# Optimization experiments

Measured on AMD Instinct MI355X. Metric: run time of the kernel, lower is better.

Reference implementation:

```python
import jax, jax.numpy as jnp
import numpy as np
import math

B, S, D, L, FF = 16, 2048, 512, 4, 2048
VOCAB, ATTR_VOCAB, MAXPOS = 33, 608, 2048
EPS = 1e-5


def layernorm(x, w, b):
    mu = jnp.mean(x, axis=-1, keepdims=True)
    var = jnp.mean(jnp.square(x - mu), axis=-1, keepdims=True)
    return (x - mu) * jax.lax.rsqrt(var + EPS) * w + b


def setup_inputs() -> dict:
    key = jax.random.key(0)
    ks = jax.random.split(key, 16)
    std = 0.02
    return {
        "input_ids": jax.random.randint(ks[0], (B, S), 0, VOCAB),
        "combined_indices": jax.random.randint(ks[1], (B,), 0, ATTR_VOCAB),
        "attention_mask": jnp.ones((B, S), dtype=jnp.float32),
        "tok_emb": jax.random.normal(ks[2], (VOCAB, D), jnp.float32) * std,
        "pos_emb": jax.random.normal(ks[3], (MAXPOS, D), jnp.float32) * std,
        "attr_emb": jax.random.normal(ks[4], (ATTR_VOCAB, D), jnp.float32) * std,
        "ln_w": jnp.ones((L, D), jnp.float32),
        "ln_b": jnp.zeros((L, D), jnp.float32),
        "w1": jax.random.normal(ks[5], (L, D, FF), jnp.float32) * std,
        "b1": jnp.zeros((L, FF), jnp.float32),
        "w2": jax.random.normal(ks[6], (L, FF, D), jnp.float32) * std,
        "b2": jnp.zeros((L, D), jnp.float32),
        "out_w": jax.random.normal(ks[7], (D, VOCAB), jnp.float32) * std,
        "out_b": jnp.zeros((VOCAB,), jnp.float32),
    }


def reference(input_ids, combined_indices, attention_mask, tok_emb, pos_emb,
              attr_emb, ln_w, ln_b, w1, b1, w2, b2, out_w, out_b):
    scale = 1.0 / math.sqrt(D)
    # embeddings: token + position + per-example attribute (broadcast over seq)
    x = tok_emb[input_ids] + pos_emb[jnp.arange(S)][None, :, :] \
        + attr_emb[combined_indices][:, None, :]
    mask_add = (1.0 - attention_mask)[:, None, :] * -1e9  # [B,1,S]
    for l in range(L):
        h = layernorm(x, ln_w[l], ln_b[l])                 # shared LN params used twice
        scores = jnp.einsum('bsd,btd->bst', h, h) * scale + mask_add
        probs = jax.nn.softmax(scores, axis=-1)            # dropout=0 (eval)
        attn = jnp.einsum('bst,btd->bsd', probs, h) + x    # residual
        n2 = layernorm(attn, ln_w[l], ln_b[l])
        ff = jax.nn.gelu(n2 @ w1[l] + b1[l], approximate=False) @ w2[l] + b2[l]
        x = ff + attn
    return x @ out_w + out_b
```

## Files before the change

### kernel.cpp

```cpp
#include <hip/hip_runtime.h>
#include <hip/hip_bf16.h>
#include <cmath>

#define B_ 16
#define S_ 2048
#define D_ 512
#define L_ 4
#define FF_ 2048
#define V_ 33

typedef unsigned short u16;
typedef __attribute__((ext_vector_type(8))) short bf16x8;
typedef __attribute__((ext_vector_type(4))) float f32x4;

__device__ __forceinline__ u16 f2bf(float f) {
    unsigned x = __float_as_uint(f);
    unsigned r = (x + 0x7fffu + ((x >> 16) & 1u)) >> 16;
    return (u16)r;
}
__device__ __forceinline__ float bf2f(u16 u) { return __uint_as_float(((unsigned)u) << 16); }

__device__ __forceinline__ float wave_sum(float v) {
#pragma unroll
    for (int o = 32; o; o >>= 1) v += __shfl_xor(v, o);
    return v;
}

__device__ __forceinline__ void gload16(const u16* g, u16* l) {
    __builtin_amdgcn_global_load_lds((const __attribute__((address_space(1))) void*)g,
                                     (__attribute__((address_space(3))) void*)l, 16, 0, 0);
}

__device__ __forceinline__ uint4 pack8(const u16* ov) {
    uint4 p;
    p.x = (unsigned)ov[0] | ((unsigned)ov[1] << 16);
    p.y = (unsigned)ov[2] | ((unsigned)ov[3] << 16);
    p.z = (unsigned)ov[4] | ((unsigned)ov[5] << 16);
    p.w = (unsigned)ov[6] | ((unsigned)ov[7] << 16);
    return p;
}

__global__ __launch_bounds__(256) void embed_kernel(
    const int* __restrict__ ids, const int* __restrict__ attr,
    const float* __restrict__ tok, const float* __restrict__ pos,
    const float* __restrict__ attre, u16* __restrict__ x)
{
    int idx = blockIdx.x * 256 + threadIdx.x;
    const int total = B_ * S_ * (D_ / 8);
    if (idx >= total) return;
    int d8 = idx & (D_ / 8 - 1);
    int bs = idx >> 6;
    int s  = bs & (S_ - 1);
    int b  = bs >> 11;
    int id = ids[bs];
    int a  = attr[b];
    const float4* t4 = (const float4*)(tok   + (size_t)id * D_) + d8 * 2;
    const float4* p4 = (const float4*)(pos   + (size_t)s  * D_) + d8 * 2;
    const float4* a4 = (const float4*)(attre + (size_t)a  * D_) + d8 * 2;
    u16 ov[8];
#pragma unroll
    for (int h = 0; h < 2; h++) {
        float4 t = t4[h], p = p4[h], at = a4[h];
        ov[h * 4 + 0] = f2bf(t.x + p.x + at.x);
        ov[h * 4 + 1] = f2bf(t.y + p.y + at.y);
        ov[h * 4 + 2] = f2bf(t.z + p.z + at.z);
        ov[h * 4 + 3] = f2bf(t.w + p.w + at.w);
    }
    *(uint4*)(x + (size_t)idx * 8) = pack8(ov);
}

__global__ __launch_bounds__(256) void ln_kernel(
    const u16* __restrict__ in, u16* __restrict__ out,
    const float* __restrict__ w, const float* __restrict__ b, int rows)
{
    int gw = (int)((blockIdx.x * 256 + threadIdx.x) >> 6);
    int lane = threadIdx.x & 63;
    if (gw >= rows) return;
    uint4 pk = *(const uint4*)(in + (size_t)gw * D_ + lane * 8);
    float xv[8];
    xv[0] = bf2f((u16)(pk.x & 0xffff)); xv[1] = bf2f((u16)(pk.x >> 16));
    xv[2] = bf2f((u16)(pk.y & 0xffff)); xv[3] = bf2f((u16)(pk.y >> 16));
    xv[4] = bf2f((u16)(pk.z & 0xffff)); xv[5] = bf2f((u16)(pk.z >> 16));
    xv[6] = bf2f((u16)(pk.w & 0xffff)); xv[7] = bf2f((u16)(pk.w >> 16));
    float s = 0.f;
#pragma unroll
    for (int k = 0; k < 8; k++) s += xv[k];
    s = wave_sum(s);
    float mu = s * (1.f / D_);
    float q = 0.f;
#pragma unroll
    for (int k = 0; k < 8; k++) { float d = xv[k] - mu; q += d * d; }
    q = wave_sum(q);
    float rs = rsqrtf(q * (1.f / D_) + 1e-5f);
    const float4* w4 = (const float4*)w;
    const float4* b4 = (const float4*)b;
    float4 w0 = w4[lane * 2], w1v = w4[lane * 2 + 1];
    float4 b0 = b4[lane * 2], b1v = b4[lane * 2 + 1];
    float wv[8] = {w0.x, w0.y, w0.z, w0.w, w1v.x, w1v.y, w1v.z, w1v.w};
    float bv[8] = {b0.x, b0.y, b0.z, b0.w, b1v.x, b1v.y, b1v.z, b1v.w};
    u16 ov[8];
#pragma unroll
    for (int k = 0; k < 8; k++) ov[k] = f2bf((xv[k] - mu) * rs * wv[k] + bv[k]);
    *(uint4*)(out + (size_t)gw * D_ + lane * 8) = pack8(ov);
}

#define LTS 66
__global__ __launch_bounds__(1024) void lnT_kernel(
    const u16* __restrict__ in, u16* __restrict__ h, u16* __restrict__ hT,
    const float* __restrict__ w, const float* __restrict__ b)
{
    __shared__ u16 tile[512 * LTS];
    const int tid = threadIdx.x, lane = tid & 63, wv = tid >> 6;
    const int rb = blockIdx.x;
    const int z  = rb >> 5;
    const int s0 = (rb & 31) * 64;

    float wv8[8], bv8[8];
#pragma unroll
    for (int k = 0; k < 8; k++) {
        wv8[k] = w[k * 64 + lane];
        bv8[k] = b[k * 64 + lane];
    }

#pragma unroll
    for (int i = 0; i < 4; i++) {
        const int rl = wv * 4 + i;
        const size_t grow = (size_t)rb * 64 + rl;
        const u16* xr = in + grow * D_;
        float xv[8];
#pragma unroll
        for (int k = 0; k < 8; k++) xv[k] = bf2f(xr[k * 64 + lane]);
        float s = 0.f;
#pragma unroll
        for (int k = 0; k < 8; k++) s += xv[k];
        s = wave_sum(s);
        float mu = s * (1.f / D_);
        float q = 0.f;
#pragma unroll
        for (int k = 0; k < 8; k++) { float d = xv[k] - mu; q += d * d; }
        q = wave_sum(q);
        float rs = rsqrtf(q * (1.f / D_) + 1e-5f);
        u16* hr = h + grow * D_;
#pragma unroll
        for (int k = 0; k < 8; k++) {
            u16 v = f2bf((xv[k] - mu) * rs * wv8[k] + bv8[k]);
            hr[k * 64 + lane] = v;
            tile[(k * 64 + lane) * LTS + rl] = v;
        }
    }
    __syncthreads();
    u16* hb = hT + (size_t)z * S_ * D_;
#pragma unroll
    for (int it = 0; it < 4; it++) {
        int idx = it * 1024 + tid;
        int d = idx >> 3, sg = (idx & 7) << 3;
        u16 v[8];
#pragma unroll
        for (int i = 0; i < 8; i++) v[i] = tile[d * LTS + sg + i];
        *(uint4*)(hb + (size_t)d * S_ + s0 + sg) = pack8(v);
    }
}

__device__ __forceinline__ void ld2(const float* p, int idx, u16& a, u16& b) {
    float2 v = ((const float2*)p)[idx];
    a = f2bf(v.x); b = f2bf(v.y);
}

__global__ void transpose64(const float* __restrict__ in, u16* __restrict__ out,
                            int R, int C, size_t sIn, size_t sOut)
{
    __shared__ u16 tile[64][66];
    const float* ip = in + (size_t)blockIdx.z * sIn;
    u16* op = out + (size_t)blockIdx.z * sOut;
    const int tx = threadIdx.x, ty = threadIdx.y;
#pragma unroll
    for (int i = 0; i < 8; i++) {
        int r = blockIdx.y * 64 + ty + i * 8;
        u16 a, b;
        ld2(ip + (size_t)r * C, blockIdx.x * 32 + tx, a, b);
        tile[tx * 2 + 0][ty + i * 8] = a;
        tile[tx * 2 + 1][ty + i * 8] = b;
    }
    __syncthreads();
#pragma unroll
    for (int i = 0; i < 8; i++) {
        int ocl = ty + i * 8;
        int oc  = blockIdx.x * 64 + ocl;
        unsigned w = (unsigned)tile[ocl][tx * 2] | ((unsigned)tile[ocl][tx * 2 + 1] << 16);
        ((unsigned*)(op + (size_t)oc * R + blockIdx.y * 64))[tx] = w;
    }
}

enum { E_PV = 1, E_GELU = 2, E_FF2 = 3 };

template <int EPI>
__global__ __launch_bounds__(256) void gemm_nt(
    const u16* __restrict__ A, size_t sAz, int lda,
    const u16* __restrict__ B, size_t sBz, int ldb,
    u16* Cb, size_t sCz, int ldc,
    int K,
    const u16* resid, size_t sRz,
    const float* __restrict__ bias,
    const float* __restrict__ aux, int b0)
{
    __shared__ __align__(16) u16 ldsA[128 * 64];
    __shared__ __align__(16) u16 ldsB[128 * 64];
    __shared__ float l2[EPI == E_PV ? 128 : 1][2];

    const int gx = gridDim.x, gy = gridDim.y;
    const int nwg = gx * gy * gridDim.z;
    int lid = blockIdx.x + gx * (blockIdx.y + gy * blockIdx.z);
    {
        const int q = nwg >> 3, r = nwg & 7;
        const int xcd = lid & 7, idx = lid >> 3;
        lid = (xcd < r ? xcd * (q + 1) : r * (q + 1) + (xcd - r) * q) + idx;
    }
    const int bx = lid % gx;
    const int t2 = lid / gx;
    const int by = t2 % gy;
    const int z  = t2 / gy;

    A += (size_t)z * sAz;
    B += (size_t)z * sBz;
    const size_t coff = (size_t)z * sCz;
    const int brow = by * 128, bcol = bx * 128;
    const int tid = threadIdx.x, lane = tid & 63, wid = tid >> 6;
    const int wr = wid >> 1, wc = wid & 1;

    if constexpr (EPI == E_PV) {
        const int nrows = b0;
        const int base = z * S_ + brow;
        const int r = tid >> 1, ih = (tid & 1) << 4;
        float s = 0.f;
#pragma unroll
        for (int i = 0; i < 16; i++)
            s += aux[(size_t)(ih + i) * nrows + base + r];
        l2[r][tid & 1] = s;
    }

    f32x4 acc[4][4];
#pragma unroll
    for (int m = 0; m < 4; m++)
#pragma unroll
        for (int n = 0; n < 4; n++) acc[m][n] = 0.0f;

    const int lg   = lane >> 3;
    const int srow = wid * 8 + lg;
    const int skk  = ((lane & 7) ^ lg) << 3;
    const int l15 = lane & 15, l7 = lane & 7, kh = lane >> 4;

    for (int k0 = 0; k0 < K; k0 += 64) {
        __syncthreads();
#pragma unroll
        for (int r = 0; r < 4; r++) {
            const u16* ga = A + (size_t)(brow + r * 32 + srow) * lda + (k0 + skk);
            const u16* gb = B + (size_t)(bcol + r * 32 + srow) * ldb + (k0 + skk);
            gload16(ga, &ldsA[r * 2048 + wid * 512]);
            gload16(gb, &ldsB[r * 2048 + wid * 512]);
        }
        __syncthreads();
#pragma unroll
        for (int kk = 0; kk < 64; kk += 32) {
            const int kc = (kk >> 3) + kh;
            const int kswz = ((kc ^ l7) << 3);
            bf16x8 af[4], bfv[4];
#pragma unroll
            for (int m = 0; m < 4; m++)
                af[m] = *(const bf16x8*)&ldsA[(wr * 64 + m * 16 + l15) * 64 + kswz];
#pragma unroll
            for (int n = 0; n < 4; n++)
                bfv[n] = *(const bf16x8*)&ldsB[(wc * 64 + n * 16 + l15) * 64 + kswz];
#pragma unroll
            for (int m = 0; m < 4; m++)
#pragma unroll
                for (int n = 0; n < 4; n++)
                    acc[m][n] = __builtin_amdgcn_mfma_f32_16x16x32_bf16(af[m], bfv[n], acc[m][n], 0, 0, 0);
        }
    }

#pragma unroll
    for (int m = 0; m < 4; m++)
#pragma unroll
        for (int n = 0; n < 4; n++) {
            int rowb = brow + wr * 64 + m * 16 + ((lane >> 4) << 2);
            int col  = bcol + wc * 64 + n * 16 + l15;
#pragma unroll
            for (int j = 0; j < 4; j++) {
                int row = rowb + j;
                float v = acc[m][n][j];
                size_t off = coff + (size_t)row * ldc + col;
                if constexpr (EPI == E_PV) {
                    int rl = row - brow;
                    float lv = l2[rl][0] + l2[rl][1];
                    Cb[off] = f2bf(v / lv +
                                   bf2f(resid[(size_t)z * sRz + (size_t)row * ldc + col]));
                } else if constexpr (EPI == E_GELU) {
                    float t = v + bias[col];
                    Cb[off] = f2bf(0.5f * t * (1.f + erff(t * 0.70710678118f)));
                } else {
                    Cb[off] = f2bf(v + bias[col] +
                                   bf2f(resid[(size_t)row * ldc + col]));
                }
            }
        }
}

__global__ __launch_bounds__(256) void gemm_sc(
    const u16* __restrict__ h, u16* __restrict__ P,
    const float* __restrict__ mask, int b0, float scale,
    float* __restrict__ psum, int nbatch)
{
    __shared__ __align__(16) u16 ldsbuf[2][128 * 64];
    u16* ldsA = ldsbuf[0];
    u16* ldsB = ldsbuf[1];
    u16* mt   = &ldsbuf[0][0];

    const int nwg = 136 * nbatch;
    int lid = blockIdx.x + 136 * blockIdx.z;
    {
        const int q = nwg >> 3, r = nwg & 7;
        const int xcd = lid & 7, idx = lid >> 3;
        lid = (xcd < r ? xcd * (q + 1) : r * (q + 1) + (xcd - r) * q) + idx;
    }
    int t = lid % 136;
    const int z = lid / 136;
    int by = 0;
#pragma unroll 1
    while (t >= 16 - by) { t -= 16 - by; by++; }
    const int bx = by + t;

    const u16* A = h + (size_t)z * S_ * D_;
    const size_t coff = (size_t)z * S_ * S_;
    const int brow = by * 128, bcol = bx * 128;
    const int tid = threadIdx.x, lane = tid & 63, wid = tid >> 6;
    const int wr = wid >> 1, wc = wid & 1;

    f32x4 acc[4][4];
#pragma unroll
    for (int m = 0; m < 4; m++)
#pragma unroll
        for (int n = 0; n < 4; n++) acc[m][n] = 0.0f;

    const int lg   = lane >> 3;
    const int srow = wid * 8 + lg;
    const int skk  = ((lane & 7) ^ lg) << 3;
    const int l15 = lane & 15, l7 = lane & 7, kh = lane >> 4;

    for (int k0 = 0; k0 < D_; k0 += 64) {
        __syncthreads();
#pragma unroll
        for (int r = 0; r < 4; r++) {
            const u16* ga = A + (size_t)(brow + r * 32 + srow) * D_ + (k0 + skk);
            const u16* gb = A + (size_t)(bcol + r * 32 + srow) * D_ + (k0 + skk);
            gload16(ga, &ldsA[r * 2048 + wid * 512]);
            gload16(gb, &ldsB[r * 2048 + wid * 512]);
        }
        __syncthreads();
#pragma unroll
        for (int kk = 0; kk < 64; kk += 32) {
            const int kc = (kk >> 3) + kh;
            const int kswz = ((kc ^ l7) << 3);
            bf16x8 af[4], bfv[4];
#pragma unroll
            for (int m = 0; m < 4; m++)
                af[m] = *(const bf16x8*)&ldsA[(wr * 64 + m * 16 + l15) * 64 + kswz];
#pragma unroll
            for (int n = 0; n < 4; n++)
                bfv[n] = *(const bf16x8*)&ldsB[(wc * 64 + n * 16 + l15) * 64 + kswz];
#pragma unroll
            for (int m = 0; m < 4; m++)
#pragma unroll
                for (int n = 0; n < 4; n++)
                    acc[m][n] = __builtin_amdgcn_mfma_f32_16x16x32_bf16(af[m], bfv[n], acc[m][n], 0, 0, 0);
        }
    }

    const float* mrow = mask + (size_t)(b0 + z) * S_;
    const int nrows = nbatch * S_;

    float rsum[4][4];
#pragma unroll
    for (int m = 0; m < 4; m++)
#pragma unroll
        for (int j = 0; j < 4; j++) rsum[m][j] = 0.f;

#pragma unroll
    for (int m = 0; m < 4; m++)
#pragma unroll
        for (int n = 0; n < 4; n++) {
            int rowb = brow + wr * 64 + m * 16 + (kh << 2);
            int col  = bcol + wc * 64 + n * 16 + l15;
            float madd_c = (1.f - mrow[col]) * -1e9f;
#pragma unroll
            for (int j = 0; j < 4; j++) {
                int row = rowb + j;
                float ev = __expf(acc[m][n][j] * scale + madd_c);
                P[coff + (size_t)row * S_ + col] = f2bf(ev);
                rsum[m][j] += ev;
            }
        }
#pragma unroll
    for (int m = 0; m < 4; m++) {
        int rowl = brow + wr * 64 + m * 16 + (kh << 2);
#pragma unroll
        for (int j = 0; j < 4; j++) {
            float s = rsum[m][j];
            s += __shfl_xor(s, 1);
            s += __shfl_xor(s, 2);
            s += __shfl_xor(s, 4);
            s += __shfl_xor(s, 8);
            if (l15 == 0)
                psum[(size_t)(bx * 2 + wc) * nrows + (size_t)z * S_ + rowl + j] = s;
        }
    }

    if (bx != by) {
#pragma unroll 1
        for (int rnd = 0; rnd < 2; rnd++) {
            __syncthreads();
            if (wc == rnd) {
#pragma unroll
                for (int n = 0; n < 4; n++) {
                    float csum = 0.f;
                    const int mrow_l = n * 16 + l15;
#pragma unroll
                    for (int m = 0; m < 4; m++) {
                        const int lr = wr * 64 + m * 16 + (kh << 2);
                        u16 e2[4];
#pragma unroll
                        for (int j = 0; j < 4; j++) {
                            float madd_r = (1.f - mrow[brow + lr + j]) * -1e9f;
                            float em = __expf(acc[m][n][j] * scale + madd_r);
                            csum += em;
                            e2[j] = f2bf(em);
                        }
                        unsigned* m32 = (unsigned*)&mt[mrow_l * 136 + lr];
                        m32[0] = (unsigned)e2[0] | ((unsigned)e2[1] << 16);
                        m32[1] = (unsigned)e2[2] | ((unsigned)e2[3] << 16);
                    }
                    csum += __shfl_xor(csum, 16);
                    csum += __shfl_xor(csum, 32);
                    if (lane < 16)
                        psum[(size_t)(by * 2 + wr) * nrows + (size_t)z * S_ +
                             bcol + rnd * 64 + n * 16 + lane] = csum;
                }
            }
            __syncthreads();
#pragma unroll 1
            for (int i = tid; i < 64 * 16; i += 256) {
                int rr = i >> 4, c16 = (i & 15) << 3;
                u16 v[8];
#pragma unroll
                for (int q = 0; q < 8; q++) v[q] = mt[rr * 136 + c16 + q];
                *(uint4*)(P + coff + (size_t)(bcol + rnd * 64 + rr) * S_ + brow + c16) = pack8(v);
            }
        }
    }
}

__global__ __launch_bounds__(256) void wtb_kernel(
    const float* __restrict__ W, u16* __restrict__ WTb)
{
    int i = blockIdx.x * 256 + threadIdx.x;
    if (i >= 64 * 512) return;
    int n = i >> 9, k = i & 511;
    WTb[i] = f2bf(n < V_ ? W[k * V_ + n] : 0.f);
}

__global__ __launch_bounds__(256) void outproj_mfma(
    const u16* __restrict__ x, const u16* __restrict__ WTb,
    const float* __restrict__ bias, float* __restrict__ out)
{
    __shared__ __align__(16) u16 ldsA[128 * 64];
    __shared__ __align__(16) u16 ldsB[64 * 64];
    __shared__ float obuf[128][34];
    const int brow = blockIdx.x * 128;
    const int tid = threadIdx.x, lane = tid & 63, wid = tid >> 6;
    const int wr = wid >> 1, wc = wid & 1;
    const int l15 = lane & 15, l7 = lane & 7, kh = lane >> 4;
    const int lg = lane >> 3, srow = wid * 8 + lg;
    const int skk = ((lane & 7) ^ lg) << 3;

    f32x4 acc[4][2];
#pragma unroll
    for (int m = 0; m < 4; m++)
#pragma unroll
        for (int n = 0; n < 2; n++) acc[m][n] = 0.0f;

    for (int k0 = 0; k0 < 512; k0 += 64) {
        __syncthreads();
#pragma unroll
        for (int r = 0; r < 2; r++)
            gload16(WTb + (size_t)(r * 32 + srow) * 512 + (k0 + skk),
                    &ldsB[r * 2048 + wid * 512]);
#pragma unroll
        for (int r = 0; r < 4; r++)
            gload16(x + (size_t)(brow + r * 32 + srow) * 512 + (k0 + skk),
                    &ldsA[r * 2048 + wid * 512]);
        __syncthreads();
#pragma unroll
        for (int kk = 0; kk < 64; kk += 32) {
            const int kc = (kk >> 3) + kh;
            const int kswz = ((kc ^ l7) << 3);
            bf16x8 af[4], bfv[2];
#pragma unroll
            for (int m = 0; m < 4; m++)
                af[m] = *(const bf16x8*)&ldsA[(wr * 64 + m * 16 + l15) * 64 + kswz];
#pragma unroll
            for (int n = 0; n < 2; n++)
                bfv[n] = *(const bf16x8*)&ldsB[(wc * 32 + n * 16 + l15) * 64 + kswz];
#pragma unroll
            for (int m = 0; m < 4; m++)
#pragma unroll
                for (int n = 0; n < 2; n++)
                    acc[m][n] = __builtin_amdgcn_mfma_f32_16x16x32_bf16(af[m], bfv[n], acc[m][n], 0, 0, 0);
        }
    }

#pragma unroll
    for (int m = 0; m < 4; m++)
#pragma unroll
        for (int n = 0; n < 2; n++) {
            int rowl = wr * 64 + m * 16 + ((lane >> 4) << 2);
            int col  = wc * 32 + n * 16 + l15;
            if (col < V_) {
#pragma unroll
                for (int j = 0; j < 4; j++)
                    obuf[rowl + j][col] = acc[m][n][j] + bias[col];
            }
        }
    __syncthreads();
    float* ob = out + (size_t)brow * V_;
#pragma unroll 1
    for (int i = tid; i < 128 * V_; i += 256)
        ob[i] = obuf[i / V_][i % V_];
}

extern "C" void kernel_launch(void* const* d_in, const int* in_sizes, int n_in,
                              void* d_out, int out_size, void* d_ws, size_t ws_size,
                              hipStream_t stream)
{
    const int*   input_ids = (const int*)d_in[0];
    const int*   comb      = (const int*)d_in[1];
    const float* amask     = (const float*)d_in[2];
    const float* tok       = (const float*)d_in[3];
    const float* pos       = (const float*)d_in[4];
    const float* attre     = (const float*)d_in[5];
    const float* ln_w      = (const float*)d_in[6];
    const float* ln_b      = (const float*)d_in[7];
    const float* w1        = (const float*)d_in[8];
    const float* b1        = (const float*)d_in[9];
    const float* w2        = (const float*)d_in[10];
    const float* b2        = (const float*)d_in[11];
    const float* out_w     = (const float*)d_in[12];
    const float* out_b     = (const float*)d_in[13];
    float* out = (float*)d_out;
    (void)in_sizes; (void)n_in; (void)out_size;

    int NB_A, RC;
    if      (ws_size >= 300000000ULL) { NB_A = 16; RC = 32768; }
    else if (ws_size >= 180000000ULL) { NB_A = 8;  RC = 16384; }
    else if (ws_size >= 120000000ULL) { NB_A = 4;  RC = 8192;  }
    else                              { NB_A = 2;  RC = 4096;  }
    const int HR = NB_A * S_;

    unsigned char* ws = (unsigned char*)d_ws;
    size_t off = 0;
    auto carve = [&](size_t bytes) {
        void* p = ws + off;
        off += (bytes + 255) & ~(size_t)255;
        return p;
    };
    u16* x      = (u16*)carve((size_t)B_ * S_ * D_ * 2);
    u16* w1t    = (u16*)carve((size_t)L_ * D_ * FF_ * 2);
    u16* w2t    = (u16*)carve((size_t)L_ * D_ * FF_ * 2);
    u16* h      = (u16*)carve((size_t)HR * D_ * 2);
    u16* hT     = (u16*)carve((size_t)NB_A * S_ * D_ * 2);
    float* psum = (float*)carve((size_t)NB_A * S_ * 32 * 4);
    u16* WTb    = (u16*)carve((size_t)64 * 512 * 2);
    size_t scP_bytes  = (size_t)NB_A * S_ * S_ * 2;
    size_t tbuf_bytes = (size_t)RC * FF_ * 2;
    void* un = carve(scP_bytes > tbuf_bytes ? scP_bytes : tbuf_bytes);
    u16* scP  = (u16*)un;
    u16* tbuf = (u16*)un;

    const float scl = 1.0f / sqrtf((float)D_);
    const int nG = B_ / NB_A;
    const int nC = (B_ * S_) / RC;

    embed_kernel<<<(B_ * S_ * (D_ / 8)) / 256, 256, 0, stream>>>(input_ids, comb, tok, pos, attre, x);
    transpose64<<<dim3(FF_ / 64, D_ / 64, L_), dim3(32, 8), 0, stream>>>(
        w1, w1t, D_, FF_, (size_t)D_ * FF_, (size_t)FF_ * D_);
    transpose64<<<dim3(D_ / 64, FF_ / 64, L_), dim3(32, 8), 0, stream>>>(
        w2, w2t, FF_, D_, (size_t)FF_ * D_, (size_t)D_ * FF_);
    wtb_kernel<<<128, 256, 0, stream>>>(out_w, WTb);

    for (int l = 0; l < L_; l++) {
        const float* lw = ln_w + l * D_;
        const float* lb = ln_b + l * D_;

        for (int g = 0; g < nG; g++) {
            u16* xg = x + (size_t)g * NB_A * S_ * D_;
            lnT_kernel<<<(NB_A * S_) / 64, 1024, 0, stream>>>(xg, h, hT, lw, lb);
            gemm_sc<<<dim3(136, 1, NB_A), 256, 0, stream>>>(
                h, scP, amask, g * NB_A, scl, psum, NB_A);
            gemm_nt<E_PV><<<dim3(D_ / 128, S_ / 128, NB_A), 256, 0, stream>>>(
                scP, (size_t)S_ * S_, S_,
                hT, (size_t)S_ * D_, S_,
                xg, (size_t)S_ * D_, D_,
                S_, xg, (size_t)S_ * D_, nullptr, psum, NB_A * S_);
        }

        for (int c = 0; c < nC; c++) {
            size_t roff = (size_t)c * RC;
            ln_kernel<<<RC / 4, 256, 0, stream>>>(x + roff * D_, h, lw, lb, RC);
            gemm_nt<E_GELU><<<dim3(FF_ / 128, RC / 128, 1), 256, 0, stream>>>(
                h, 0, D_,
                w1t + (size_t)l * FF_ * D_, 0, D_,
                tbuf, 0, FF_,
                D_, nullptr, 0, b1 + l * FF_, nullptr, 0);
            gemm_nt<E_FF2><<<dim3(D_ / 128, RC / 128, 1), 256, 0, stream>>>(
                tbuf, 0, FF_,
                w2t + (size_t)l * D_ * FF_, 0, FF_,
                x + roff * D_, 0, D_,
                FF_, x + roff * D_, 0, b2 + l * D_, nullptr, 0);
        }
    }

    outproj_mfma<<<(B_ * S_) / 128, 256, 0, stream>>>(x, WTb, out_b, out);
}
```

Before: 1.905 ms.

## Fuse second LayerNorm into FF1 GEMM prologue

Drops the standalone LayerNorm kernel before the first feed-forward GEMM and builds a dedicated FF1 GEMM that computes per-row mean and variance itself. It then normalizes the A tile on the fly while staging it into LDS. This removes one kernel launch and the write and re-read of the normalized activation buffer. In exchange, every column block recomputes row statistics and the normalization (16x redundant across FF/128 blocks). The A tile is now loaded synchronously through registers rather than with async global-to-LDS loads, and variance uses the one-pass E[x²]-mu² form, which is less accurate.

```diff
diff --git a/kernel.cpp b/kernel.cpp
--- a/kernel.cpp
+++ b/kernel.cpp
@@ -38,6 +38,12 @@
     p.z = (unsigned)ov[4] | ((unsigned)ov[5] << 16);
     p.w = (unsigned)ov[6] | ((unsigned)ov[7] << 16);
     return p;
+}
+__device__ __forceinline__ void unpack8(uint4 p, float* v) {
+    v[0] = bf2f((u16)(p.x & 0xffff)); v[1] = bf2f((u16)(p.x >> 16));
+    v[2] = bf2f((u16)(p.y & 0xffff)); v[3] = bf2f((u16)(p.y >> 16));
+    v[4] = bf2f((u16)(p.z & 0xffff)); v[5] = bf2f((u16)(p.z >> 16));
+    v[6] = bf2f((u16)(p.w & 0xffff)); v[7] = bf2f((u16)(p.w >> 16));
 }
 
 __global__ __launch_bounds__(256) void embed_kernel(
@@ -69,41 +75,6 @@
     *(uint4*)(x + (size_t)idx * 8) = pack8(ov);
 }
 
-__global__ __launch_bounds__(256) void ln_kernel(
-    const u16* __restrict__ in, u16* __restrict__ out,
-    const float* __restrict__ w, const float* __restrict__ b, int rows)
-{
-    int gw = (int)((blockIdx.x * 256 + threadIdx.x) >> 6);
-    int lane = threadIdx.x & 63;
-    if (gw >= rows) return;
-    uint4 pk = *(const uint4*)(in + (size_t)gw * D_ + lane * 8);
-    float xv[8];
-    xv[0] = bf2f((u16)(pk.x & 0xffff)); xv[1] = bf2f((u16)(pk.x >> 16));
-    xv[2] = bf2f((u16)(pk.y & 0xffff)); xv[3] = bf2f((u16)(pk.y >> 16));
-    xv[4] = bf2f((u16)(pk.z & 0xffff)); xv[5] = bf2f((u16)(pk.z >> 16));
-    xv[6] = bf2f((u16)(pk.w & 0xffff)); xv[7] = bf2f((u16)(pk.w >> 16));
-    float s = 0.f;
-#pragma unroll
-    for (int k = 0; k < 8; k++) s += xv[k];
-    s = wave_sum(s);
-    float mu = s * (1.f / D_);
-    float q = 0.f;
-#pragma unroll
-    for (int k = 0; k < 8; k++) { float d = xv[k] - mu; q += d * d; }
-    q = wave_sum(q);
-    float rs = rsqrtf(q * (1.f / D_) + 1e-5f);
-    const float4* w4 = (const float4*)w;
-    const float4* b4 = (const float4*)b;
-    float4 w0 = w4[lane * 2], w1v = w4[lane * 2 + 1];
-    float4 b0 = b4[lane * 2], b1v = b4[lane * 2 + 1];
-    float wv[8] = {w0.x, w0.y, w0.z, w0.w, w1v.x, w1v.y, w1v.z, w1v.w};
-    float bv[8] = {b0.x, b0.y, b0.z, b0.w, b1v.x, b1v.y, b1v.z, b1v.w};
-    u16 ov[8];
-#pragma unroll
-    for (int k = 0; k < 8; k++) ov[k] = f2bf((xv[k] - mu) * rs * wv[k] + bv[k]);
-    *(uint4*)(out + (size_t)gw * D_ + lane * 8) = pack8(ov);
-}
-
 #define LTS 66
 __global__ __launch_bounds__(1024) void lnT_kernel(
     const u16* __restrict__ in, u16* __restrict__ h, u16* __restrict__ hT,
@@ -191,7 +162,7 @@
     }
 }
 
-enum { E_PV = 1, E_GELU = 2, E_FF2 = 3 };
+enum { E_PV = 1, E_FF2 = 3 };
 
 template <int EPI>
 __global__ __launch_bounds__(256) void gemm_nt(
@@ -294,13 +265,125 @@
                     float lv = l2[rl][0] + l2[rl][1];
                     Cb[off] = f2bf(v / lv +
                                    bf2f(resid[(size_t)z * sRz + (size_t)row * ldc + col]));
-                } else if constexpr (EPI == E_GELU) {
-                    float t = v + bias[col];
-                    Cb[off] = f2bf(0.5f * t * (1.f + erff(t * 0.70710678118f)));
                 } else {
                     Cb[off] = f2bf(v + bias[col] +
                                    bf2f(resid[(size_t)row * ldc + col]));
                 }
+            }
+        }
+}
+
+__global__ __launch_bounds__(256) void gemm_ff1(
+    const u16* __restrict__ x, const u16* __restrict__ w1t,
+    u16* __restrict__ tbuf, const float* __restrict__ bias,
+    const float* __restrict__ lnw, const float* __restrict__ lnb)
+{
+    __shared__ __align__(16) u16 ldsA[128 * 64];
+    __shared__ __align__(16) u16 ldsB[128 * 64];
+    __shared__ float wln[512], bln[512];
+
+    const int gx = gridDim.x, gy = gridDim.y;
+    const int nwg = gx * gy;
+    int lid = blockIdx.x + gx * blockIdx.y;
+    {
+        const int q = nwg >> 3, r = nwg & 7;
+        const int xcd = lid & 7, idx = lid >> 3;
+        lid = (xcd < r ? xcd * (q + 1) : r * (q + 1) + (xcd - r) * q) + idx;
+    }
+    const int bx = lid % gx;
+    const int by = lid / gx;
+    const int brow = by * 128, bcol = bx * 128;
+    const int tid = threadIdx.x, lane = tid & 63, wid = tid >> 6;
+    const int wr = wid >> 1, wc = wid & 1;
+
+    if (tid < 128) {
+        float4 wv = ((const float4*)lnw)[tid];
+        float4 bv = ((const float4*)lnb)[tid];
+        *(float4*)&wln[tid * 4] = wv;
+        *(float4*)&bln[tid * 4] = bv;
+    }
+
+    const int ar = tid >> 1, ah = (tid & 1) * 32;
+    const u16* xrow = x + (size_t)(brow + ar) * D_;
+    float sum = 0.f, sq = 0.f;
+#pragma unroll
+    for (int k0 = 0; k0 < 512; k0 += 64) {
+#pragma unroll
+        for (int j = 0; j < 4; j++) {
+            float v[8];
+            unpack8(*(const uint4*)(xrow + k0 + ah + j * 8), v);
+#pragma unroll
+            for (int e = 0; e < 8; e++) { sum += v[e]; sq += v[e] * v[e]; }
+        }
+    }
+    sum += __shfl_xor(sum, 1);
+    sq  += __shfl_xor(sq, 1);
+    const float mu = sum * (1.f / D_);
+    const float var = fmaxf(sq * (1.f / D_) - mu * mu, 0.f);
+    const float rs = rsqrtf(var + 1e-5f);
+
+    f32x4 acc[4][4];
+#pragma unroll
+    for (int m = 0; m < 4; m++)
+#pragma unroll
+        for (int n = 0; n < 4; n++) acc[m][n] = 0.0f;
+
+    const int lg   = lane >> 3;
+    const int srow = wid * 8 + lg;
+    const int skk  = ((lane & 7) ^ lg) << 3;
+    const int l15 = lane & 15, l7 = lane & 7, kh = lane >> 4;
+    const int a7 = ar & 7;
+
+    for (int k0 = 0; k0 < 512; k0 += 64) {
+        __syncthreads();
+#pragma unroll
+        for (int r = 0; r < 4; r++)
+            gload16(w1t + (size_t)(bcol + r * 32 + srow) * D_ + (k0 + skk),
+                    &ldsB[r * 2048 + wid * 512]);
+#pragma unroll
+        for (int j = 0; j < 4; j++) {
+            float v[8];
+            unpack8(*(const uint4*)(xrow + k0 + ah + j * 8), v);
+            u16 t[8];
+#pragma unroll
+            for (int e = 0; e < 8; e++) {
+                int c = k0 + ah + j * 8 + e;
+                t[e] = f2bf((v[e] - mu) * rs * wln[c] + bln[c]);
+            }
+            int kc = (ah >> 3) + j;
+            *(uint4*)&ldsA[ar * 64 + ((kc ^ a7) << 3)] = pack8(t);
+        }
+        __syncthreads();
+#pragma unroll
+        for (int kk = 0; kk < 64; kk += 32) {
+            const int kc = (kk >> 3) + kh;
+            const int kswz = ((kc ^ l7) << 3);
+            bf16x8 af[4], bfv[4];
+#pragma unroll
+            for (int m = 0; m < 4; m++)
+                af[m] = *(const bf16x8*)&ldsA[(wr * 64 + m * 16 + l15) * 64 + kswz];
+#pragma unroll
+            for (int n = 0; n < 4; n++)
+                bfv[n] = *(const bf16x8*)&ldsB[(wc * 64 + n * 16 + l15) * 64 + kswz];
+#pragma unroll
+            for (int m = 0; m < 4; m++)
+#pragma unroll
+                for (int n = 0; n < 4; n++)
+                    acc[m][n] = __builtin_amdgcn_mfma_f32_16x16x32_bf16(af[m], bfv[n], acc[m][n], 0, 0, 0);
+        }
+    }
+
+#pragma unroll
+    for (int m = 0; m < 4; m++)
+#pragma unroll
+        for (int n = 0; n < 4; n++) {
+            int rowb = brow + wr * 64 + m * 16 + ((lane >> 4) << 2);
+            int col  = bcol + wc * 64 + n * 16 + l15;
+#pragma unroll
+            for (int j = 0; j < 4; j++) {
+                float t = acc[m][n][j] + bias[col];
+                tbuf[(size_t)(rowb + j) * FF_ + col] =
+                    f2bf(0.5f * t * (1.f + erff(t * 0.70710678118f)));
             }
         }
 }
@@ -613,12 +696,9 @@
 
         for (int c = 0; c < nC; c++) {
             size_t roff = (size_t)c * RC;
-            ln_kernel<<<RC / 4, 256, 0, stream>>>(x + roff * D_, h, lw, lb, RC);
-            gemm_nt<E_GELU><<<dim3(FF_ / 128, RC / 128, 1), 256, 0, stream>>>(
-                h, 0, D_,
-                w1t + (size_t)l * FF_ * D_, 0, D_,
-                tbuf, 0, FF_,
-                D_, nullptr, 0, b1 + l * FF_, nullptr, 0);
+            gemm_ff1<<<dim3(FF_ / 128, RC / 128), 256, 0, stream>>>(
+                x + roff * D_, w1t + (size_t)l * FF_ * D_,
+                tbuf, b1 + l * FF_, lw, lb);
             gemm_nt<E_FF2><<<dim3(D_ / 128, RC / 128, 1), 256, 0, stream>>>(
                 tbuf, 0, FF_,
                 w2t + (size_t)l * D_ * FF_, 0, FF_,
```

Measured after the change: 2.225 ms. +16.8%, slower.
